# Performance work log

Measured on AMD Instinct MI355X. Metric: run time of the kernel, lower is better.

Reference implementation:

```python
import jax, jax.numpy as jnp
import numpy as np

N, E, IN_DIM, H, C = 100000, 1600000, 128, 4, 64
NEG_SLOPE = 0.2
BN_EPS = 1e-5


def setup_inputs() -> dict:
    key = jax.random.key(0)
    ks = jax.random.split(key, 9)
    s = 1.0 / np.sqrt(IN_DIM)
    return {
        "feature": jax.random.normal(ks[0], (N, IN_DIM), dtype=jnp.float32),
        "edge_index": jax.random.randint(ks[1], (2, E), 0, N, dtype=jnp.int64),
        "W_l": jax.random.uniform(ks[2], (IN_DIM, H * C), jnp.float32, -s, s),
        "b_l": jnp.zeros((H * C,), jnp.float32),
        "W_r": jax.random.uniform(ks[3], (IN_DIM, H * C), jnp.float32, -s, s),
        "b_r": jnp.zeros((H * C,), jnp.float32),
        "att": jax.random.normal(ks[4], (H, C), dtype=jnp.float32) * 0.1,
        "bias": jnp.zeros((H * C,), jnp.float32),
        "gamma": jnp.ones((H * C,), jnp.float32),
        "beta": jnp.zeros((H * C,), jnp.float32),
    }


def reference(feature, edge_index, W_l, b_l, W_r, b_r, att, bias, gamma, beta):
    n = feature.shape[0]
    # add self loops (add_self_loops=True)
    loops = jnp.arange(n, dtype=edge_index.dtype)
    src = jnp.concatenate([edge_index[0], loops])
    dst = jnp.concatenate([edge_index[1], loops])
    # GATv2: separate source/target linear projections -> [N, H, C]
    x_l = (feature @ W_l + b_l).reshape(n, H, C)
    x_r = (feature @ W_r + b_r).reshape(n, H, C)
    # per-edge attention score: a^T LeakyReLU(x_l[src] + x_r[dst])  [Etot, H]
    e = jax.nn.leaky_relu(x_l[src] + x_r[dst], NEG_SLOPE)
    alpha = jnp.einsum('ehc,hc->eh', e, att)
    # segment softmax over incoming edges per target node
    amax = jax.ops.segment_max(alpha, dst, num_segments=n)  # [N, H]
    alpha = jnp.exp(alpha - amax[dst])
    denom = jax.ops.segment_sum(alpha, dst, num_segments=n)  # [N, H]
    alpha = alpha / (denom[dst] + 1e-16)
    # weighted scatter-aggregate of source messages
    out = jax.ops.segment_sum(x_l[src] * alpha[:, :, None], dst, num_segments=n)
    out = out.reshape(n, H * C) + bias  # concat=True
    # BatchNorm1d (training: batch statistics over nodes)
    mean = out.mean(axis=0)
    var = out.var(axis=0)
    out = (out - mean) / jnp.sqrt(var + BN_EPS) * gamma + beta
    return jax.nn.relu(out)
```

## Files before the change

kernel.cpp:

```cpp
#include <hip/hip_runtime.h>
#include <cstdint>

#define IN_DIM 128
#define HC 256
#define NEG_SLOPE 0.2f
#define BN_EPS 1e-5f
#define LOG2E 1.44269504088896340736f

typedef short bf16x8 __attribute__((ext_vector_type(8)));
typedef float f32x4 __attribute__((ext_vector_type(4)));

#define EXP2F(x) __builtin_amdgcn_exp2f(x)

__device__ __forceinline__ unsigned short f2bf(float f) {
    union { float f; unsigned int u; } v; v.f = f;
    unsigned int r = (v.u + 0x7FFFu + ((v.u >> 16) & 1u)) >> 16;
    return (unsigned short)r;
}
__device__ __forceinline__ float bf2f(unsigned short h) {
    union { unsigned int u; float f; } v; v.u = ((unsigned int)h) << 16;
    return v.f;
}

template<int CTRL>
__device__ __forceinline__ float dppadd(float x) {
    int y = __builtin_amdgcn_update_dpp(0, __builtin_bit_cast(int, x), CTRL, 0xF, 0xF, true);
    return x + __builtin_bit_cast(float, y);
}
__device__ __forceinline__ float red16(float p) {
    p = dppadd<0xB1>(p);
    p = dppadd<0x4E>(p);
    p = dppadd<0x124>(p);
    p = dppadd<0x128>(p);
    return p;
}

__device__ __forceinline__ void unpk(ushort4 u, float* f) {
    f[0] = bf2f(u.x); f[1] = bf2f(u.y); f[2] = bf2f(u.z); f[3] = bf2f(u.w);
}
__device__ __forceinline__ float esc(const float* f, float x0, float x1, float x2, float x3,
                                     float4 a) {
    float z0 = f[0] + x0, z1 = f[1] + x1, z2 = f[2] + x2, z3 = f[3] + x3;
    float p = a.x * fmaxf(z0, NEG_SLOPE * z0);
    p = fmaf(a.y, fmaxf(z1, NEG_SLOPE * z1), p);
    p = fmaf(a.z, fmaxf(z2, NEG_SLOPE * z2), p);
    p = fmaf(a.w, fmaxf(z3, NEG_SLOPE * z3), p);
    return p;
}

__global__ __launch_bounds__(64) void cast_w(
    const float* __restrict__ Wl, const float* __restrict__ Wr,
    unsigned short* __restrict__ Wfrag)
{
    int j = blockIdx.x >> 2;
    int kk = blockIdx.x & 3;
    int l = threadIdx.x;
    int col = j * 16 + (l & 15);
    const float* W = (col < 256) ? Wl : Wr;
    int c = col & 255;
    unsigned short tmp[8];
#pragma unroll
    for (int m = 0; m < 8; ++m) {
        int k = kk * 32 + ((l >> 4) << 3) + m;
        tmp[m] = f2bf(W[(size_t)k * 256 + c]);
    }
    ulonglong2* dst = (ulonglong2*)(Wfrag + ((size_t)(j * 4 + kk) * 64 + l) * 8);
    *dst = *(ulonglong2*)tmp;
}

__global__ __launch_bounds__(256) void cast_a(
    const float* __restrict__ A, unsigned short* __restrict__ Afrag, int n)
{
    int i = blockIdx.x;
    int kk = threadIdx.x >> 6;
    int l = threadIdx.x & 63;
    int row = i * 16 + (l & 15);
    int k0 = kk * 32 + ((l >> 4) << 3);
    float4 f0 = make_float4(0.f, 0.f, 0.f, 0.f), f1 = f0;
    if (row < n) {
        const float* p = A + (size_t)row * IN_DIM + k0;
        f0 = *(const float4*)p;
        f1 = *(const float4*)(p + 4);
    }
    unsigned short tmp[8];
    tmp[0] = f2bf(f0.x); tmp[1] = f2bf(f0.y); tmp[2] = f2bf(f0.z); tmp[3] = f2bf(f0.w);
    tmp[4] = f2bf(f1.x); tmp[5] = f2bf(f1.y); tmp[6] = f2bf(f1.z); tmp[7] = f2bf(f1.w);
    ulonglong2* dst = (ulonglong2*)(Afrag + ((size_t)(i * 4 + kk) * 64 + l) * 8);
    *dst = *(ulonglong2*)tmp;
}

__global__ __launch_bounds__(256) void gemm_mfma(
    const unsigned short* __restrict__ Afrag, const unsigned short* __restrict__ Wfrag,
    const float* __restrict__ bl, const float* __restrict__ br,
    unsigned short* __restrict__ xl, unsigned short* __restrict__ xr,
    int n, int ntiles)
{
    int i = blockIdx.x * 4 + (threadIdx.x >> 6);
    if (i >= ntiles) return;
    int l = threadIdx.x & 63;

    const bf16x8* av = (const bf16x8*)(Afrag + ((size_t)i * 4 * 64 + l) * 8);
    bf16x8 a0 = av[0 * 64], a1 = av[1 * 64], a2 = av[2 * 64], a3 = av[3 * 64];

    const bf16x8* wv = (const bf16x8*)Wfrag + l;
    int cl = l & 15;
    int rbase = i * 16 + ((l >> 4) << 2);

#pragma unroll 4
    for (int j = 0; j < 32; ++j) {
        const bf16x8* bp = wv + (size_t)j * 4 * 64;
        f32x4 acc = {0.f, 0.f, 0.f, 0.f};
        acc = __builtin_amdgcn_mfma_f32_16x16x32_bf16(a0, bp[0 * 64], acc, 0, 0, 0);
        acc = __builtin_amdgcn_mfma_f32_16x16x32_bf16(a1, bp[1 * 64], acc, 0, 0, 0);
        acc = __builtin_amdgcn_mfma_f32_16x16x32_bf16(a2, bp[2 * 64], acc, 0, 0, 0);
        acc = __builtin_amdgcn_mfma_f32_16x16x32_bf16(a3, bp[3 * 64], acc, 0, 0, 0);

        int col = j * 16 + cl;
        unsigned short* X = (col < 256) ? xl : xr;
        int c = col & 255;
        float b = (col < 256) ? bl[c] : br[c];
#pragma unroll
        for (int q = 0; q < 4; ++q) {
            int row = rbase + q;
            if (row < n) X[(size_t)row * HC + c] = f2bf(acc[q] + b);
        }
    }
}

__global__ void hist_rank_kernel(const int* __restrict__ ei, int* __restrict__ cnt,
                                 int* __restrict__ rank, int E, int n)
{
    int total = E + n;
    for (int e = blockIdx.x * blockDim.x + threadIdx.x; e < total;
         e += gridDim.x * blockDim.x) {
        int dst = (e < E) ? ei[(size_t)E + e] : (e - E);
        rank[e] = atomicAdd(&cnt[dst], 1);
    }
}

#define SCAN_BLOCKS 256

__global__ __launch_bounds__(256) void scan_phaseA(const int* __restrict__ cnt,
                                                   int* __restrict__ blocksums,
                                                   int n, int ept)
{
    __shared__ int red[256];
    int t = threadIdx.x;
    int g = blockIdx.x * 256 + t;
    int beg = g * ept, end = min(beg + ept, n);
    int s = 0;
    for (int i = beg; i < end; ++i) s += cnt[i];
    red[t] = s;
    __syncthreads();
    for (int d = 128; d > 0; d >>= 1) {
        if (t < d) red[t] += red[t + d];
        __syncthreads();
    }
    if (t == 0) blocksums[blockIdx.x] = red[0];
}

__global__ __launch_bounds__(256) void scan_phaseB(const int* __restrict__ blocksums,
                                                   int* __restrict__ blockoffs,
                                                   int* __restrict__ off, int n)
{
    __shared__ int sums[256];
    int t = threadIdx.x;
    sums[t] = blocksums[t];
    __syncthreads();
    for (int d = 1; d < 256; d <<= 1) {
        int v = (t >= d) ? sums[t - d] : 0;
        __syncthreads();
        sums[t] += v;
        __syncthreads();
    }
    blockoffs[t] = (t == 0) ? 0 : sums[t - 1];
    if (t == 255) off[n] = sums[255];
}

__global__ __launch_bounds__(256) void scan_phaseC(const int* __restrict__ cnt,
                                                   const int* __restrict__ blockoffs,
                                                   int* __restrict__ off,
                                                   int n, int ept)
{
    __shared__ int sums[256];
    int t = threadIdx.x;
    int g = blockIdx.x * 256 + t;
    int beg = g * ept, end = min(beg + ept, n);
    int s = 0;
    for (int i = beg; i < end; ++i) s += cnt[i];
    sums[t] = s;
    __syncthreads();
    for (int d = 1; d < 256; d <<= 1) {
        int v = (t >= d) ? sums[t - d] : 0;
        __syncthreads();
        sums[t] += v;
        __syncthreads();
    }
    int run = blockoffs[blockIdx.x] + ((t == 0) ? 0 : sums[t - 1]);
    for (int i = beg; i < end; ++i) {
        int c = cnt[i];
        off[i] = run;
        run += c;
    }
}

__global__ void fill_kernel(const int* __restrict__ ei, const int* __restrict__ rank,
                            const int* __restrict__ off, int* __restrict__ csr_boff,
                            int E, int n)
{
    int total = E + n;
    for (int e = blockIdx.x * blockDim.x + threadIdx.x; e < total;
         e += gridDim.x * blockDim.x) {
        int src, dst;
        if (e < E) { src = ei[e]; dst = ei[(size_t)E + e]; }
        else       { src = dst = e - E; }
        int pos = off[dst] + rank[e];
        csr_boff[pos] = src << 9;
    }
}

__global__ __launch_bounds__(256) void gat_agg(
    const unsigned short* __restrict__ xl, const unsigned short* __restrict__ xr,
    const int* __restrict__ csr_boff, const int* __restrict__ off,
    const float* __restrict__ att, const float* __restrict__ bias,
    float* __restrict__ out, int n)
{
    int d = (blockIdx.x * blockDim.x + threadIdx.x) >> 6;
    int lane = threadIdx.x & 63;
    if (d >= n) return;

    const char* xlc = (const char*)xl;
    int lo8 = lane << 3;
    ushort4 xru = ((const ushort4*)xr)[(size_t)d * 64 + lane];
    float xr0 = bf2f(xru.x), xr1 = bf2f(xru.y), xr2 = bf2f(xru.z), xr3 = bf2f(xru.w);
    float4 att4 = *(const float4*)(att + 4 * lane);
    att4.x *= LOG2E; att4.y *= LOG2E; att4.z *= LOG2E; att4.w *= LOG2E;

    int beg = __builtin_amdgcn_readfirstlane(off[d]);
    int end = __builtin_amdgcn_readfirstlane(off[d + 1]);
    float m = -INFINITY;
    float lsum = 0.f;
    float ax = 0.f, ay = 0.f, az = 0.f, aw = 0.f;

    int i = beg;
    for (; i + 3 < end; i += 4) {
        int b0 = __builtin_amdgcn_readfirstlane(csr_boff[i]);
        int b1 = __builtin_amdgcn_readfirstlane(csr_boff[i + 1]);
        int b2 = __builtin_amdgcn_readfirstlane(csr_boff[i + 2]);
        int b3 = __builtin_amdgcn_readfirstlane(csr_boff[i + 3]);
        ushort4 u0 = *(const ushort4*)(xlc + b0 + lo8);
        ushort4 u1 = *(const ushort4*)(xlc + b1 + lo8);
        ushort4 u2 = *(const ushort4*)(xlc + b2 + lo8);
        ushort4 u3 = *(const ushort4*)(xlc + b3 + lo8);
        float f0[4], f1[4], f2[4], f3[4];
        unpk(u0, f0); unpk(u1, f1); unpk(u2, f2); unpk(u3, f3);

        float p0 = esc(f0, xr0, xr1, xr2, xr3, att4);
        float p1 = esc(f1, xr0, xr1, xr2, xr3, att4);
        float p2 = esc(f2, xr0, xr1, xr2, xr3, att4);
        float p3 = esc(f3, xr0, xr1, xr2, xr3, att4);

        p0 = dppadd<0xB1>(p0);  p1 = dppadd<0xB1>(p1);  p2 = dppadd<0xB1>(p2);  p3 = dppadd<0xB1>(p3);
        p0 = dppadd<0x4E>(p0);  p1 = dppadd<0x4E>(p1);  p2 = dppadd<0x4E>(p2);  p3 = dppadd<0x4E>(p3);
        p0 = dppadd<0x124>(p0); p1 = dppadd<0x124>(p1); p2 = dppadd<0x124>(p2); p3 = dppadd<0x124>(p3);
        p0 = dppadd<0x128>(p0); p1 = dppadd<0x128>(p1); p2 = dppadd<0x128>(p2); p3 = dppadd<0x128>(p3);

        float mx = fmaxf(fmaxf(p0, p1), fmaxf(p2, p3));
        if (mx > m) {
            float sc = EXP2F(m - mx);
            ax *= sc; ay *= sc; az *= sc; aw *= sc; lsum *= sc;
            m = mx;
        }
        float e0 = EXP2F(p0 - m), e1 = EXP2F(p1 - m);
        float e2 = EXP2F(p2 - m), e3 = EXP2F(p3 - m);
        ax = fmaf(e0, f0[0], fmaf(e1, f1[0], fmaf(e2, f2[0], fmaf(e3, f3[0], ax))));
        ay = fmaf(e0, f0[1], fmaf(e1, f1[1], fmaf(e2, f2[1], fmaf(e3, f3[1], ay))));
        az = fmaf(e0, f0[2], fmaf(e1, f1[2], fmaf(e2, f2[2], fmaf(e3, f3[2], az))));
        aw = fmaf(e0, f0[3], fmaf(e1, f1[3], fmaf(e2, f2[3], fmaf(e3, f3[3], aw))));
        lsum += (e0 + e1) + (e2 + e3);
    }
    for (; i < end; ++i) {
        int b0 = __builtin_amdgcn_readfirstlane(csr_boff[i]);
        ushort4 u0 = *(const ushort4*)(xlc + b0 + lo8);
        float f0[4];
        unpk(u0, f0);
        float p0 = esc(f0, xr0, xr1, xr2, xr3, att4);
        p0 = red16(p0);
        if (p0 > m) {
            float sc = EXP2F(m - p0);
            ax *= sc; ay *= sc; az *= sc; aw *= sc; lsum *= sc;
            m = p0;
        }
        float e0 = EXP2F(p0 - m);
        ax = fmaf(e0, f0[0], ax); ay = fmaf(e0, f0[1], ay);
        az = fmaf(e0, f0[2], az); aw = fmaf(e0, f0[3], aw);
        lsum += e0;
    }

    float inv = 1.f / (lsum + 1e-16f);
    float4 b4 = *(const float4*)(bias + 4 * lane);
    float4 o;
    o.x = fmaf(ax, inv, b4.x); o.y = fmaf(ay, inv, b4.y);
    o.z = fmaf(az, inv, b4.z); o.w = fmaf(aw, inv, b4.w);
    *(float4*)(out + (size_t)d * HC + 4 * lane) = o;
}

#define NB_BN 1024
__global__ __launch_bounds__(256) void bn_partial(const float* __restrict__ out,
                                                  float* __restrict__ partials, int n)
{
    int c = threadIdx.x;
    int b = blockIdx.x;
    int chunk = (n + NB_BN - 1) / NB_BN;
    int beg = b * chunk;
    int end = min(beg + chunk, n);
    float s = 0.f, s2 = 0.f;
    for (int r = beg; r < end; ++r) {
        float v = out[(size_t)r * HC + c];
        s += v; s2 += v * v;
    }
    partials[(size_t)b * 512 + c] = s;
    partials[(size_t)b * 512 + 256 + c] = s2;
}

__global__ __launch_bounds__(256) void bn_final(const float* __restrict__ partials,
                                                float* __restrict__ stats, int n)
{
    int c = blockIdx.x;
    int t = threadIdx.x;
    float s = 0.f, s2 = 0.f;
    for (int b = t; b < NB_BN; b += 256) {
        s  += partials[(size_t)b * 512 + c];
        s2 += partials[(size_t)b * 512 + 256 + c];
    }
    __shared__ float rs[256], rs2[256];
    rs[t] = s; rs2[t] = s2;
    __syncthreads();
    for (int d = 128; d > 0; d >>= 1) {
        if (t < d) { rs[t] += rs[t + d]; rs2[t] += rs2[t + d]; }
        __syncthreads();
    }
    if (t == 0) {
        float mean = rs[0] / (float)n;
        float var = rs2[0] / (float)n - mean * mean;
        stats[c] = mean;
        stats[256 + c] = rsqrtf(var + BN_EPS);
    }
}

__global__ void bn_apply(float* __restrict__ out, const float* __restrict__ stats,
                         const float* __restrict__ gamma, const float* __restrict__ beta,
                         long long total4)
{
    long long stride = (long long)gridDim.x * blockDim.x;
    for (long long i = blockIdx.x * (long long)blockDim.x + threadIdx.x; i < total4;
         i += stride) {
        int cb = ((int)(i & 63)) * 4;
        float4 v = ((const float4*)out)[i];
        float4 o;
        o.x = fmaxf(0.f, (v.x - stats[cb + 0]) * stats[256 + cb + 0] * gamma[cb + 0] + beta[cb + 0]);
        o.y = fmaxf(0.f, (v.y - stats[cb + 1]) * stats[256 + cb + 1] * gamma[cb + 1] + beta[cb + 1]);
        o.z = fmaxf(0.f, (v.z - stats[cb + 2]) * stats[256 + cb + 2] * gamma[cb + 2] + beta[cb + 2]);
        o.w = fmaxf(0.f, (v.w - stats[cb + 3]) * stats[256 + cb + 3] * gamma[cb + 3] + beta[cb + 3]);
        ((float4*)out)[i] = o;
    }
}

extern "C" void kernel_launch(void* const* d_in, const int* in_sizes, int n_in,
                              void* d_out, int out_size, void* d_ws, size_t ws_size,
                              hipStream_t stream)
{
    const float* feature = (const float*)d_in[0];
    const int* ei        = (const int*)d_in[1];
    const float* Wl   = (const float*)d_in[2];
    const float* bl   = (const float*)d_in[3];
    const float* Wr   = (const float*)d_in[4];
    const float* br   = (const float*)d_in[5];
    const float* att  = (const float*)d_in[6];
    const float* bias = (const float*)d_in[7];
    const float* gamma = (const float*)d_in[8];
    const float* beta  = (const float*)d_in[9];

    const int n = in_sizes[0] / IN_DIM;
    const int E = in_sizes[1] / 2;
    const int Etot = E + n;
    const int ntiles = (n + 15) / 16;

    char* ws = (char*)d_ws;
    size_t o = 0;
    auto carve = [&](size_t bytes) -> void* {
        void* p = ws + o; o = (o + bytes + 15) & ~(size_t)15; return p;
    };
    unsigned short* xl    = (unsigned short*)carve((size_t)n * HC * sizeof(short));
    unsigned short* xr    = (unsigned short*)carve((size_t)n * HC * sizeof(short));
    unsigned short* Afrag = (unsigned short*)carve((size_t)ntiles * 4 * 64 * 8 * sizeof(short));
    unsigned short* Wfrag = (unsigned short*)carve((size_t)32 * 4 * 64 * 8 * sizeof(short));
    int*   csr_boff = (int*)carve((size_t)Etot * sizeof(int));
    int*   rank    = (int*)carve((size_t)Etot * sizeof(int));
    int*   cnt     = (int*)carve((size_t)n * sizeof(int));
    int*   off     = (int*)carve((size_t)(n + 1) * sizeof(int));
    int*   blocksums = (int*)carve(SCAN_BLOCKS * sizeof(int));
    int*   blockoffs = (int*)carve(SCAN_BLOCKS * sizeof(int));
    float* partials = (float*)carve((size_t)NB_BN * 512 * sizeof(float));
    float* stats   = (float*)carve(512 * sizeof(float));
    float* outf = (float*)d_out;

    if (o > ws_size) return;

    cast_w<<<128, 64, 0, stream>>>(Wl, Wr, Wfrag);
    cast_a<<<ntiles, 256, 0, stream>>>(feature, Afrag, n);
    gemm_mfma<<<(ntiles + 3) / 4, 256, 0, stream>>>(Afrag, Wfrag, bl, br, xl, xr, n, ntiles);

    (void)hipMemsetAsync(cnt, 0, (size_t)n * sizeof(int), stream);
    hist_rank_kernel<<<2048, 256, 0, stream>>>(ei, cnt, rank, E, n);
    int ept = (n + SCAN_BLOCKS * 256 - 1) / (SCAN_BLOCKS * 256);
    scan_phaseA<<<SCAN_BLOCKS, 256, 0, stream>>>(cnt, blocksums, n, ept);
    scan_phaseB<<<1, 256, 0, stream>>>(blocksums, blockoffs, off, n);
    scan_phaseC<<<SCAN_BLOCKS, 256, 0, stream>>>(cnt, blockoffs, off, n, ept);
    fill_kernel<<<2048, 256, 0, stream>>>(ei, rank, off, csr_boff, E, n);

    int agg_blocks = (n + 3) / 4;
    gat_agg<<<agg_blocks, 256, 0, stream>>>(xl, xr, csr_boff, off, att, bias, outf, n);

    bn_partial<<<NB_BN, 256, 0, stream>>>(outf, partials, n);
    bn_final<<<256, 256, 0, stream>>>(partials, stats, n);
    long long total4 = (long long)n * (HC / 4);
    bn_apply<<<4096, 256, 0, stream>>>(outf, stats, gamma, beta, total4);
}
```

Measured before the change: 390.9 us.

## Merge independent prep kernels into two heterogeneous launches for concurrent execution

The histogram/rank pass is combined with the weight and feature bf16 casts into one kernel, and the CSR fill is combined with the MFMA projection GEMM into another, with each block choosing its role from its block index. This cuts the number of launches and lets the atomic-bound graph passes run alongside the bandwidth- and compute-bound GEMM work, where before they ran one after another. Grid sizes for the histogram and fill roles also shrink (1536 and 512 blocks in place of 2048), which may change how those loops balance across the device.

New measurement: 391.6 us. About the same (+0.2%).

```diff
diff --git a/kernel.cpp b/kernel.cpp
--- a/kernel.cpp
+++ b/kernel.cpp
@@ -6,6 +6,10 @@
 #define NEG_SLOPE 0.2f
 #define BN_EPS 1e-5f
 #define LOG2E 1.44269504088896340736f
+
+#define B_HIST 1536
+#define B_CW 32
+#define B_FILL 512
 
 typedef short bf16x8 __attribute__((ext_vector_type(8)));
 typedef float f32x4 __attribute__((ext_vector_type(4)));
@@ -48,93 +52,53 @@
     return p;
 }
 
-__global__ __launch_bounds__(64) void cast_w(
+__global__ __launch_bounds__(256) void phase1(
+    const float* __restrict__ F, unsigned short* __restrict__ Afrag,
     const float* __restrict__ Wl, const float* __restrict__ Wr,
-    unsigned short* __restrict__ Wfrag)
-{
-    int j = blockIdx.x >> 2;
-    int kk = blockIdx.x & 3;
-    int l = threadIdx.x;
-    int col = j * 16 + (l & 15);
-    const float* W = (col < 256) ? Wl : Wr;
-    int c = col & 255;
-    unsigned short tmp[8];
+    unsigned short* __restrict__ Wfrag,
+    const int* __restrict__ ei, int* __restrict__ cnt, int* __restrict__ rank,
+    int E, int n, int ntiles)
+{
+    int b = blockIdx.x;
+    if (b < B_HIST) {
+        int total = E + n;
+        for (int e = b * 256 + threadIdx.x; e < total; e += B_HIST * 256) {
+            int dst = (e < E) ? ei[(size_t)E + e] : (e - E);
+            rank[e] = atomicAdd(&cnt[dst], 1);
+        }
+    } else if (b < B_HIST + B_CW) {
+        int ob = (b - B_HIST) * 4 + (threadIdx.x >> 6);
+        int j = ob >> 2;
+        int kk = ob & 3;
+        int l = threadIdx.x & 63;
+        int col = j * 16 + (l & 15);
+        const float* W = (col < 256) ? Wl : Wr;
+        int c = col & 255;
+        unsigned short tmp[8];
 #pragma unroll
-    for (int m = 0; m < 8; ++m) {
-        int k = kk * 32 + ((l >> 4) << 3) + m;
-        tmp[m] = f2bf(W[(size_t)k * 256 + c]);
-    }
-    ulonglong2* dst = (ulonglong2*)(Wfrag + ((size_t)(j * 4 + kk) * 64 + l) * 8);
-    *dst = *(ulonglong2*)tmp;
-}
-
-__global__ __launch_bounds__(256) void cast_a(
-    const float* __restrict__ A, unsigned short* __restrict__ Afrag, int n)
-{
-    int i = blockIdx.x;
-    int kk = threadIdx.x >> 6;
-    int l = threadIdx.x & 63;
-    int row = i * 16 + (l & 15);
-    int k0 = kk * 32 + ((l >> 4) << 3);
-    float4 f0 = make_float4(0.f, 0.f, 0.f, 0.f), f1 = f0;
-    if (row < n) {
-        const float* p = A + (size_t)row * IN_DIM + k0;
-        f0 = *(const float4*)p;
-        f1 = *(const float4*)(p + 4);
-    }
-    unsigned short tmp[8];
-    tmp[0] = f2bf(f0.x); tmp[1] = f2bf(f0.y); tmp[2] = f2bf(f0.z); tmp[3] = f2bf(f0.w);
-    tmp[4] = f2bf(f1.x); tmp[5] = f2bf(f1.y); tmp[6] = f2bf(f1.z); tmp[7] = f2bf(f1.w);
-    ulonglong2* dst = (ulonglong2*)(Afrag + ((size_t)(i * 4 + kk) * 64 + l) * 8);
-    *dst = *(ulonglong2*)tmp;
-}
-
-__global__ __launch_bounds__(256) void gemm_mfma(
-    const unsigned short* __restrict__ Afrag, const unsigned short* __restrict__ Wfrag,
-    const float* __restrict__ bl, const float* __restrict__ br,
-    unsigned short* __restrict__ xl, unsigned short* __restrict__ xr,
-    int n, int ntiles)
-{
-    int i = blockIdx.x * 4 + (threadIdx.x >> 6);
-    if (i >= ntiles) return;
-    int l = threadIdx.x & 63;
-
-    const bf16x8* av = (const bf16x8*)(Afrag + ((size_t)i * 4 * 64 + l) * 8);
-    bf16x8 a0 = av[0 * 64], a1 = av[1 * 64], a2 = av[2 * 64], a3 = av[3 * 64];
-
-    const bf16x8* wv = (const bf16x8*)Wfrag + l;
-    int cl = l & 15;
-    int rbase = i * 16 + ((l >> 4) << 2);
-
-#pragma unroll 4
-    for (int j = 0; j < 32; ++j) {
-        const bf16x8* bp = wv + (size_t)j * 4 * 64;
-        f32x4 acc = {0.f, 0.f, 0.f, 0.f};
-        acc = __builtin_amdgcn_mfma_f32_16x16x32_bf16(a0, bp[0 * 64], acc, 0, 0, 0);
-        acc = __builtin_amdgcn_mfma_f32_16x16x32_bf16(a1, bp[1 * 64], acc, 0, 0, 0);
-        acc = __builtin_amdgcn_mfma_f32_16x16x32_bf16(a2, bp[2 * 64], acc, 0, 0, 0);
-        acc = __builtin_amdgcn_mfma_f32_16x16x32_bf16(a3, bp[3 * 64], acc, 0, 0, 0);
-
-        int col = j * 16 + cl;
-        unsigned short* X = (col < 256) ? xl : xr;
-        int c = col & 255;
-        float b = (col < 256) ? bl[c] : br[c];
-#pragma unroll
-        for (int q = 0; q < 4; ++q) {
-            int row = rbase + q;
-            if (row < n) X[(size_t)row * HC + c] = f2bf(acc[q] + b);
-        }
-    }
-}
-
-__global__ void hist_rank_kernel(const int* __restrict__ ei, int* __restrict__ cnt,
-                                 int* __restrict__ rank, int E, int n)
-{
-    int total = E + n;
-    for (int e = blockIdx.x * blockDim.x + threadIdx.x; e < total;
-         e += gridDim.x * blockDim.x) {
-        int dst = (e < E) ? ei[(size_t)E + e] : (e - E);
-        rank[e] = atomicAdd(&cnt[dst], 1);
+        for (int m = 0; m < 8; ++m) {
+            int k = kk * 32 + ((l >> 4) << 3) + m;
+            tmp[m] = f2bf(W[(size_t)k * 256 + c]);
+        }
+        ulonglong2* dst = (ulonglong2*)(Wfrag + ((size_t)(j * 4 + kk) * 64 + l) * 8);
+        *dst = *(ulonglong2*)tmp;
+    } else {
+        int i = b - B_HIST - B_CW;
+        int kk = threadIdx.x >> 6;
+        int l = threadIdx.x & 63;
+        int row = i * 16 + (l & 15);
+        int k0 = kk * 32 + ((l >> 4) << 3);
+        float4 f0 = make_float4(0.f, 0.f, 0.f, 0.f), f1 = f0;
+        if (row < n) {
+            const float* p = F + (size_t)row * IN_DIM + k0;
+            f0 = *(const float4*)p;
+            f1 = *(const float4*)(p + 4);
+        }
+        unsigned short tmp[8];
+        tmp[0] = f2bf(f0.x); tmp[1] = f2bf(f0.y); tmp[2] = f2bf(f0.z); tmp[3] = f2bf(f0.w);
+        tmp[4] = f2bf(f1.x); tmp[5] = f2bf(f1.y); tmp[6] = f2bf(f1.z); tmp[7] = f2bf(f1.w);
+        ulonglong2* dst = (ulonglong2*)(Afrag + ((size_t)(i * 4 + kk) * 64 + l) * 8);
+        *dst = *(ulonglong2*)tmp;
     }
 }
 
@@ -204,18 +168,55 @@
     }
 }
 
-__global__ void fill_kernel(const int* __restrict__ ei, const int* __restrict__ rank,
-                            const int* __restrict__ off, int* __restrict__ csr_boff,
-                            int E, int n)
-{
-    int total = E + n;
-    for (int e = blockIdx.x * blockDim.x + threadIdx.x; e < total;
-         e += gridDim.x * blockDim.x) {
-        int src, dst;
-        if (e < E) { src = ei[e]; dst = ei[(size_t)E + e]; }
-        else       { src = dst = e - E; }
-        int pos = off[dst] + rank[e];
-        csr_boff[pos] = src << 9;
+__global__ __launch_bounds__(256) void phase2(
+    const unsigned short* __restrict__ Afrag, const unsigned short* __restrict__ Wfrag,
+    const float* __restrict__ bl, const float* __restrict__ br,
+    unsigned short* __restrict__ xl, unsigned short* __restrict__ xr,
+    const int* __restrict__ ei, const int* __restrict__ rank,
+    const int* __restrict__ off, int* __restrict__ csr_boff,
+    int E, int n, int ntiles)
+{
+    int b = blockIdx.x;
+    if (b < B_FILL) {
+        int total = E + n;
+        for (int e = b * 256 + threadIdx.x; e < total; e += B_FILL * 256) {
+            int src, dst;
+            if (e < E) { src = ei[e]; dst = ei[(size_t)E + e]; }
+            else       { src = dst = e - E; }
+            int pos = off[dst] + rank[e];
+            csr_boff[pos] = src << 9;
+        }
+    } else {
+        int i = (b - B_FILL) * 4 + (threadIdx.x >> 6);
+        if (i >= ntiles) return;
+        int l = threadIdx.x & 63;
+
+        const bf16x8* av = (const bf16x8*)(Afrag + ((size_t)i * 4 * 64 + l) * 8);
+        bf16x8 a0 = av[0 * 64], a1 = av[1 * 64], a2 = av[2 * 64], a3 = av[3 * 64];
+
+        const bf16x8* wv = (const bf16x8*)Wfrag + l;
+        int cl = l & 15;
+        int rbase = i * 16 + ((l >> 4) << 2);
+
+#pragma unroll 4
+        for (int j = 0; j < 32; ++j) {
+            const bf16x8* bp = wv + (size_t)j * 4 * 64;
+            f32x4 acc = {0.f, 0.f, 0.f, 0.f};
+            acc = __builtin_amdgcn_mfma_f32_16x16x32_bf16(a0, bp[0 * 64], acc, 0, 0, 0);
+            acc = __builtin_amdgcn_mfma_f32_16x16x32_bf16(a1, bp[1 * 64], acc, 0, 0, 0);
+            acc = __builtin_amdgcn_mfma_f32_16x16x32_bf16(a2, bp[2 * 64], acc, 0, 0, 0);
+            acc = __builtin_amdgcn_mfma_f32_16x16x32_bf16(a3, bp[3 * 64], acc, 0, 0, 0);
+
+            int col = j * 16 + cl;
+            unsigned short* X = (col < 256) ? xl : xr;
+            int c = col & 255;
+            float bv = (col < 256) ? bl[c] : br[c];
+#pragma unroll
+            for (int q = 0; q < 4; ++q) {
+                int row = rbase + q;
+                if (row < n) X[(size_t)row * HC + c] = f2bf(acc[q] + bv);
+            }
+        }
     }
 }
 
@@ -407,17 +408,18 @@
 
     if (o > ws_size) return;
 
-    cast_w<<<128, 64, 0, stream>>>(Wl, Wr, Wfrag);
-    cast_a<<<ntiles, 256, 0, stream>>>(feature, Afrag, n);
-    gemm_mfma<<<(ntiles + 3) / 4, 256, 0, stream>>>(Afrag, Wfrag, bl, br, xl, xr, n, ntiles);
-
     (void)hipMemsetAsync(cnt, 0, (size_t)n * sizeof(int), stream);
-    hist_rank_kernel<<<2048, 256, 0, stream>>>(ei, cnt, rank, E, n);
+
+    phase1<<<B_HIST + B_CW + ntiles, 256, 0, stream>>>(
+        feature, Afrag, Wl, Wr, Wfrag, ei, cnt, rank, E, n, ntiles);
+
     int ept = (n + SCAN_BLOCKS * 256 - 1) / (SCAN_BLOCKS * 256);
     scan_phaseA<<<SCAN_BLOCKS, 256, 0, stream>>>(cnt, blocksums, n, ept);
     scan_phaseB<<<1, 256, 0, stream>>>(blocksums, blockoffs, off, n);
     scan_phaseC<<<SCAN_BLOCKS, 256, 0, stream>>>(cnt, blockoffs, off, n, ept);
-    fill_kernel<<<2048, 256, 0, stream>>>(ei, rank, off, csr_boff, E, n);
+
+    phase2<<<B_FILL + (ntiles + 3) / 4, 256, 0, stream>>>(
+        Afrag, Wfrag, bl, br, xl, xr, ei, rank, off, csr_boff, E, n, ntiles);
 
     int agg_blocks = (n + 3) / 4;
     gat_agg<<<agg_blocks, 256, 0, stream>>>(xl, xr, csr_boff, off, att, bias, outf, n);
```
